# Performance work log

Measured on AMD Instinct MI355X. Metric: run time of the kernel, lower is better.

Reference implementation:

```python
import jax, jax.numpy as jnp
import numpy as np

N_QUBITS = 16
DIM = 1 << N_QUBITS
NUM_CLASSES = 23
BATCH = 64

# PauliZ sign table: wire 0 is the most-significant bit of the flattened index.
_idx = np.arange(DIM)
SIGNS = np.stack([1 - 2 * ((_idx >> (N_QUBITS - 1 - w)) & 1) for w in range(N_QUBITS)], axis=1).astype(np.float32)  # (DIM, 16)


def _rx_mat(theta):
    c = jnp.cos(theta / 2).astype(jnp.complex64)
    s = (-1j * jnp.sin(theta / 2)).astype(jnp.complex64)
    return jnp.stack([jnp.stack([c, s]), jnp.stack([s, c])])  # (2,2)


def _rot_mat(phi, theta, omega):
    ct = jnp.cos(theta / 2)
    st = jnp.sin(theta / 2)
    a = jnp.exp(-0.5j * (phi + omega)) * ct
    b = -jnp.exp(0.5j * (phi - omega)) * st
    c = jnp.exp(-0.5j * (phi - omega)) * st
    d = jnp.exp(0.5j * (phi + omega)) * ct
    return jnp.stack([jnp.stack([a, b]), jnp.stack([c, d])]).astype(jnp.complex64)


def _apply_1q(state, U, w):
    # state: (B, 2,...,2); shared 2x2 gate on wire w (axis w+1)
    st = jnp.tensordot(state, U, axes=[[w + 1], [1]])  # contracted axis moves to last
    return jnp.moveaxis(st, -1, w + 1)


def _apply_rx_batched(state, theta_b, w):
    # per-sample RX angles theta_b: (B,)
    half = theta_b / 2
    c = jnp.cos(half).astype(jnp.complex64)
    s = (-1j * jnp.sin(half)).astype(jnp.complex64)
    U = jnp.stack([jnp.stack([c, s], -1), jnp.stack([s, c], -1)], -2)  # (B,2,2)
    st = jnp.moveaxis(state, w + 1, -1)
    st = jnp.einsum('bji,b...i->b...j', U, st)
    return jnp.moveaxis(st, -1, w + 1)


def _apply_crx(state, theta, ctrl, tgt):
    s0 = jax.lax.index_in_dim(state, 0, axis=ctrl + 1, keepdims=False)
    s1 = jax.lax.index_in_dim(state, 1, axis=ctrl + 1, keepdims=False)
    tax = tgt + 1 if tgt < ctrl else tgt  # target axis after control axis removal
    U = _rx_mat(theta)
    s1 = jnp.moveaxis(jnp.tensordot(s1, U, axes=[[tax], [1]]), -1, tax)
    return jnp.stack([s0, s1], axis=ctrl + 1)


def _circuit(x, w0, x0, w1, x1):
    B = x.shape[0]
    state = jnp.zeros((B,) + (2,) * N_QUBITS, jnp.complex64)
    state = state.at[(slice(None),) + (0,) * N_QUBITS].set(1.0)
    for w, xc in ((w0, x0), (w1, x1)):
        for q in range(N_QUBITS):
            state = _apply_rx_batched(state, x[:, q], q)
        for q in range(N_QUBITS):
            state = _apply_1q(state, _rot_mat(w[q, 0], w[q, 1], w[q, 2]), q)
        for q in range(N_QUBITS):
            state = _apply_crx(state, xc[q], q, (q + 1) % N_QUBITS)
    probs = (state.real ** 2 + state.imag ** 2).reshape(B, DIM)
    return probs @ jnp.asarray(SIGNS)  # (B, 16) PauliZ expvals


def setup_inputs() -> dict:
    key = jax.random.key(0)
    ks = jax.random.split(key, 7)
    return {
        'x': jax.random.normal(ks[0], (BATCH, N_QUBITS), jnp.float32),
        'w0': jax.random.normal(ks[1], (N_QUBITS, 3), jnp.float32),
        'x0': jax.random.normal(ks[2], (N_QUBITS,), jnp.float32),
        'w1': jax.random.normal(ks[3], (N_QUBITS, 3), jnp.float32),
        'x1': jax.random.normal(ks[4], (N_QUBITS,), jnp.float32),
        'fc_w': jax.random.normal(ks[5], (NUM_CLASSES, N_QUBITS), jnp.float32) * 0.25,
        'fc_b': jax.random.normal(ks[6], (NUM_CLASSES,), jnp.float32) * 0.05,
    }


def reference(x, w0, x0, w1, x1, fc_w, fc_b):
    feats = _circuit(x, w0, x0, w1, x1)           # (B, 16)
    logits = feats @ fc_w.T + fc_b                # (B, 23)
    return jax.nn.log_softmax(logits, axis=1)
```

## Files before the change

### kernel.cpp

```cpp
#include <hip/hip_runtime.h>
#include <hip/hip_bf16.h>


#define DIM 65536
#define BATCH 64
#define PSTR 580


template<int RB>
__device__ __forceinline__ void g1q_reg(float* sr, float* si, const float* U) {
  float u00r=U[0],u00i=U[1],u01r=U[2],u01i=U[3],u10r=U[4],u10i=U[5],u11r=U[6],u11i=U[7];
#pragma unroll
  for (int k = 0; k < 8; ++k) {
    int lo = k & ((1<<RB)-1);
    int j0 = ((k >> RB) << (RB+1)) | lo;
    int j1 = j0 | (1<<RB);
    float a0r=sr[j0], a0i=si[j0], a1r=sr[j1], a1i=si[j1];
    sr[j0] = u00r*a0r - u00i*a0i + u01r*a1r - u01i*a1i;
    si[j0] = u00r*a0i + u00i*a0r + u01r*a1i + u01i*a1r;
    sr[j1] = u10r*a0r - u10i*a0i + u11r*a1r - u11i*a1i;
    si[j1] = u10r*a0i + u10i*a0r + u11r*a1i + u11i*a1r;
  }
}

template<int RB, int CB>
__device__ __forceinline__ void gsel_reg_cc(float* sr, float* si, const float* M0, const float* M1) {
  float a0=M0[0],a1=M0[1],a2=M0[2],a3=M0[3],a4=M0[4],a5=M0[5],a6=M0[6],a7=M0[7];
  float b0=M1[0],b1=M1[1],b2=M1[2],b3=M1[3],b4=M1[4],b5=M1[5],b6=M1[6],b7=M1[7];
#pragma unroll
  for (int k = 0; k < 8; ++k) {
    int lo = k & ((1<<RB)-1);
    int j0 = ((k >> RB) << (RB+1)) | lo;
    int j1 = j0 | (1<<RB);
    const bool c = ((j0 >> CB) & 1) != 0;
    float u00r=c?b0:a0, u00i=c?b1:a1, u01r=c?b2:a2, u01i=c?b3:a3;
    float u10r=c?b4:a4, u10i=c?b5:a5, u11r=c?b6:a6, u11i=c?b7:a7;
    float p0r=sr[j0], p0i=si[j0], p1r=sr[j1], p1i=si[j1];
    sr[j0] = u00r*p0r - u00i*p0i + u01r*p1r - u01i*p1i;
    si[j0] = u00r*p0i + u00i*p0r + u01r*p1i + u01i*p1r;
    sr[j1] = u10r*p0r - u10i*p0i + u11r*p1r - u11i*p1i;
    si[j1] = u10r*p0i + u10i*p0r + u11r*p1i + u11i*p1r;
  }
}

template<int RB>
__device__ __forceinline__ void gsel_reg_pred(float* sr, float* si, const float* M0,
                                              const float* M1, bool ctrl) {
  float u[8];
#pragma unroll
  for (int e = 0; e < 8; ++e) u[e] = ctrl ? M1[e] : M0[e];
  g1q_reg<RB>(sr, si, u);
}

template<int CB, int LB>
__device__ __forceinline__ void crx_reg_lane(float* sr, float* si, float c, float s) {
#pragma unroll
  for (int k = 0; k < 8; ++k) {
    int lo2 = k & ((1<<CB)-1);
    int j = ((((k >> CB) << (CB+1)) | lo2)) | (1<<CB);
    float pr = __shfl_xor(sr[j], 1<<LB, 64);
    float pi = __shfl_xor(si[j], 1<<LB, 64);
    float mr = sr[j], mi = si[j];
    sr[j] = c*mr + s*pi;
    si[j] = c*mi - s*pr;
  }
}

__device__ __forceinline__ int swz(int o) { return o ^ ((o>>4)&15) ^ ((o>>8)&15); }

__device__ __forceinline__ unsigned bfp(float r, float i) {
  unsigned ur = __float_as_uint(r), ui = __float_as_uint(i);
  ur = (ur + 0x7fffu + ((ur >> 16) & 1u)) >> 16;
  ui = (ui + 0x7fffu + ((ui >> 16) & 1u)) & 0xffff0000u;
  return (ur & 0xffffu) | ui;
}
__device__ __forceinline__ float bfr(unsigned u) { return __uint_as_float(u << 16); }
__device__ __forceinline__ float bfi(unsigned u) { return __uint_as_float(u & 0xffff0000u); }

#define MP(Pb, l, q, s) ((Pb) + (((l)*16+(q))*2+(s))*8)


__global__ __launch_bounds__(256) void pA(float2* __restrict__ pre2, float* __restrict__ P,
                                          const float* __restrict__ x, const float* __restrict__ w0,
                                          const float* __restrict__ x0, const float* __restrict__ w1,
                                          const float* __restrict__ x1, float* __restrict__ feats,
                                          int* __restrict__ ctr) {
  __shared__ float2 lds2[4096];
  int b = blockIdx.x;
  int t = threadIdx.x, lane = t & 63, wv = t >> 6;
  float* Pb = P + (size_t)b * PSTR;

  {
    float (*su)[8] = reinterpret_cast<float(*)[8]>(lds2);
    if (t < 16) feats[b*16 + t] = 0.f;
    if (t == 16) ctr[b] = 0;
    if (t < 32) {
      int l = t >> 4, q = t & 15;
      const float* W = (l ? w1 : w0) + q*3;
      float xa = 0.5f * x[b*16 + q];
      float cr = cosf(xa), sx = sinf(xa);
      float phi = W[0], th = W[1], om = W[2];
      float ct = cosf(0.5f*th), stt = sinf(0.5f*th);
      float po = 0.5f*(phi+om), pm = 0.5f*(phi-om);
      float ar =  cosf(po)*ct,  ai = -sinf(po)*ct;
      float br = -cosf(pm)*stt, bi = -sinf(pm)*stt;
      float cr2 = cosf(pm)*stt, ci2 = -sinf(pm)*stt;
      float dr =  cosf(po)*ct,  di =  sinf(po)*ct;
      float U[8];
      U[0] = ar*cr + bi*sx;   U[1] = ai*cr - br*sx;
      U[2] = ai*sx + br*cr;   U[3] = -ar*sx + bi*cr;
      U[4] = cr2*cr + di*sx;  U[5] = ci2*cr - dr*sx;
      U[6] = ci2*sx + dr*cr;  U[7] = -cr2*sx + di*cr;
      float* M0 = MP(Pb, l, q, 0);
      float* M1 = M0 + 8;
#pragma unroll
      for (int e = 0; e < 8; ++e) { M0[e] = U[e]; su[t][e] = U[e]; }
      if (q == 0) {
        float ang = l ? 0.5f*x0[15] : 0.f;
        float cg = cosf(ang), sg = sinf(ang);
        M1[0] =  cg*U[0] + sg*U[3];  M1[1] = cg*U[1] - sg*U[2];
        M1[2] =  sg*U[1] + cg*U[2];  M1[3] = -sg*U[0] + cg*U[3];
        M1[4] =  cg*U[4] + sg*U[7];  M1[5] = cg*U[5] - sg*U[6];
        M1[6] =  sg*U[5] + cg*U[6];  M1[7] = -sg*U[4] + cg*U[7];
      } else {
        float ang = 0.5f*(l ? x1[q-1] : x0[q-1]);
        float cg = cosf(ang), sg = sinf(ang);
        M1[0] = cg*U[0] + sg*U[5];  M1[1] = cg*U[1] - sg*U[4];
        M1[2] = cg*U[2] + sg*U[7];  M1[3] = cg*U[3] - sg*U[6];
        M1[4] = cg*U[4] + sg*U[1];  M1[5] = cg*U[5] - sg*U[0];
        M1[6] = cg*U[6] + sg*U[3];  M1[7] = cg*U[7] - sg*U[2];
      }
      if (t == 0) { Pb[576] = cosf(0.5f*x1[15]); Pb[577] = sinf(0.5f*x1[15]); }
    }
    __syncthreads();
    if (t == 0) {
      float T0r[8], T0i[8], T1r[8], T1i[8];
#pragma unroll
      for (int k = 0; k < 8; ++k) {
        int b2 = (k>>2)&1, b1 = (k>>1)&1, b0k = k&1;
        float xr = su[13][b2*4], xi = su[13][b2*4+1];
        float yr = su[14][b1*4], yi = su[14][b1*4+1];
        float zr = su[15][b0k*4], zi = su[15][b0k*4+1];
        float pr = xr*yr - xi*yi, pi = xr*yi + xi*yr;
        T0r[k] = pr*zr - pi*zi; T0i[k] = pr*zi + pi*zr;
      }
      float a12 = 0.5f*x0[12], c12 = cosf(a12), s12 = sinf(a12);
#pragma unroll
      for (int k = 0; k < 8; ++k) { T1r[k] = c12*T0r[k] + s12*T0i[k^4]; T1i[k] = c12*T0i[k] - s12*T0r[k^4]; }
      float a13 = 0.5f*x0[13], c13 = cosf(a13), s13 = sinf(a13);
      float n0r[8], n0i[8], n1r[8], n1i[8];
#pragma unroll
      for (int k = 0; k < 8; ++k) {
        if (k & 4) {
          n0r[k] = c13*T0r[k] + s13*T0i[k^2]; n0i[k] = c13*T0i[k] - s13*T0r[k^2];
          n1r[k] = c13*T1r[k] + s13*T1i[k^2]; n1i[k] = c13*T1i[k] - s13*T1r[k^2];
        } else { n0r[k]=T0r[k]; n0i[k]=T0i[k]; n1r[k]=T1r[k]; n1i[k]=T1i[k]; }
      }
      float a14 = 0.5f*x0[14], c14 = cosf(a14), s14 = sinf(a14);
      float Fr[2][8], Fi[2][8];
#pragma unroll
      for (int k = 0; k < 8; ++k) {
        float r0, i0, r1, i1;
        if (k & 2) {
          r0 = c14*n0r[k] + s14*n0i[k^1]; i0 = c14*n0i[k] - s14*n0r[k^1];
          r1 = c14*n1r[k] + s14*n1i[k^1]; i1 = c14*n1i[k] - s14*n1r[k^1];
        } else { r0=n0r[k]; i0=n0i[k]; r1=n1r[k]; i1=n1i[k]; }
        Fr[0][k] = r0; Fi[0][k] = i0; Fr[1][k] = r1; Fi[1][k] = i1;
      }
      const float* A = MP(Pb,0,12,0);
      const float* B = MP(Pb,0,12,1);
      float wr[2][2], wi[2][2];
      wr[0][0] = A[0]; wi[0][0] = A[1];  wr[1][0] = A[4]; wi[1][0] = A[5];
      wr[0][1] = B[0]; wi[0][1] = B[1];  wr[1][1] = B[4]; wi[1][1] = B[5];
      float* T2 = Pb + 512;
#pragma unroll
      for (int j0 = 0; j0 < 2; ++j0)
#pragma unroll
        for (int j1 = 0; j1 < 2; ++j1)
#pragma unroll
          for (int k = 0; k < 8; ++k) {
            float tr = Fr[j0][k], ti = Fi[j0][k];
            float fr = wr[j0][j1], fi = wi[j0][j1];
            T2[((j0*2 + j1)*8 + k)*2 + 0] = tr*fr - ti*fi;
            T2[((j0*2 + j1)*8 + k)*2 + 1] = tr*fi + ti*fr;
          }
    }
  }

  float sr[16], si[16];
#pragma unroll
  for (int r = 0; r < 16; ++r) { sr[r] = 0.f; si[r] = 0.f; }
  if (t == 0) sr[0] = 1.f;

  g1q_reg<3>(sr, si, MP(Pb,0,0,0));
  gsel_reg_cc<2,3>(sr, si, MP(Pb,0,1,0), MP(Pb,0,1,1));
  gsel_reg_cc<1,2>(sr, si, MP(Pb,0,2,0), MP(Pb,0,2,1));
  gsel_reg_cc<0,1>(sr, si, MP(Pb,0,3,0), MP(Pb,0,3,1));
  __syncthreads();
#pragma unroll
  for (int r = 0; r < 16; ++r) {
    int o = wv | (lane << 2) | (r << 8);
    lds2[swz(o) & 4095] = make_float2(sr[r], si[r]);
  }
  __syncthreads();
#pragma unroll
  for (int r = 0; r < 16; ++r) {
    int o = wv | (((lane>>4)&3) << 2) | (r << 4) | ((lane&15) << 8);
    float2 v = lds2[swz(o) & 4095]; sr[r] = v.x; si[r] = v.y;
  }
  gsel_reg_pred<3>(sr, si, MP(Pb,0,4,0), MP(Pb,0,4,1), (lane&1)!=0);
  gsel_reg_cc<2,3>(sr, si, MP(Pb,0,5,0), MP(Pb,0,5,1));
  gsel_reg_cc<1,2>(sr, si, MP(Pb,0,6,0), MP(Pb,0,6,1));
  gsel_reg_cc<0,1>(sr, si, MP(Pb,0,7,0), MP(Pb,0,7,1));
  __syncthreads();
#pragma unroll
  for (int r = 0; r < 16; ++r) {
    int o = wv | (((lane>>4)&3) << 2) | (r << 4) | ((lane&15) << 8);
    lds2[swz(o) & 4095] = make_float2(sr[r], si[r]);
  }
  __syncthreads();
#pragma unroll
  for (int r = 0; r < 16; ++r) {
    int o = r | (lane << 4) | (wv << 10);
    float2 v = lds2[swz(o) & 4095]; sr[r] = v.x; si[r] = v.y;
  }
  gsel_reg_pred<3>(sr, si, MP(Pb,0,8,0), MP(Pb,0,8,1), (lane&1)!=0);
  gsel_reg_cc<2,3>(sr, si, MP(Pb,0,9,0), MP(Pb,0,9,1));
  gsel_reg_cc<1,2>(sr, si, MP(Pb,0,10,0), MP(Pb,0,10,1));
  gsel_reg_cc<0,1>(sr, si, MP(Pb,0,11,0), MP(Pb,0,11,1));
#pragma unroll
  for (int r = 0; r < 16; ++r) {
    int paddr = ((lane>>4)&3) | (wv << 2) | (r << 4) | ((lane&15) << 8);
    pre2[(size_t)b*4096 + paddr] = make_float2(sr[r], si[r]);
  }
}


__global__ __launch_bounds__(512) void pB(unsigned* __restrict__ st, const float2* __restrict__ pre2,
                                          const float* __restrict__ P) {
  __shared__ float2 lds2[8192];
  int blk = blockIdx.x;
  int b = blk >> 3, m = blk & 7;
  int t = threadIdx.x, lane = t & 63, wv = t >> 6;
  const float* Pb = P + (size_t)b*PSTR;

  float sr[16], si[16];
  {
    const float4* src = (const float4*)(pre2 + (size_t)b*4096) + ((lane << 3) | ((wv&3) << 9));
    int k = ((wv>>2)&1) | ((m&3) << 1);
    const float* tf = Pb + 512 + ((((m>>2)&1)*2 + (lane&1))*8 + k)*2;
    float fr = tf[0], fi = tf[1];
#pragma unroll
    for (int g = 0; g < 8; ++g) {
      float4 v = src[g];
      sr[2*g]   = fr*v.x - fi*v.y;  si[2*g]   = fr*v.y + fi*v.x;
      sr[2*g+1] = fr*v.z - fi*v.w;  si[2*g+1] = fr*v.w + fi*v.z;
    }
  }
  gsel_reg_pred<3>(sr, si, MP(Pb,1,0,0), MP(Pb,1,0,1), ((wv>>2)&1)!=0);
  gsel_reg_cc<2,3>(sr, si, MP(Pb,1,1,0), MP(Pb,1,1,1));
  gsel_reg_cc<1,2>(sr, si, MP(Pb,1,2,0), MP(Pb,1,2,1));
  gsel_reg_cc<0,1>(sr, si, MP(Pb,1,3,0), MP(Pb,1,3,1));
#pragma unroll
  for (int r = 0; r < 16; ++r) {
    int o = (lane&63) | ((wv&3) << 6) | (r << 8) | (((wv>>2)&1) << 12);
    lds2[swz(o) & 8191] = make_float2(sr[r], si[r]);
  }
  __syncthreads();
#pragma unroll
  for (int r = 0; r < 16; ++r) {
    int o = (lane&15) | (r << 4) | (((lane>>4)&3) << 8) | ((wv&3) << 10) | (((wv>>2)&1) << 12);
    float2 v = lds2[swz(o) & 8191]; sr[r] = v.x; si[r] = v.y;
  }
  gsel_reg_pred<3>(sr, si, MP(Pb,1,4,0), MP(Pb,1,4,1), (lane&16)!=0);
  gsel_reg_cc<2,3>(sr, si, MP(Pb,1,5,0), MP(Pb,1,5,1));
  gsel_reg_cc<1,2>(sr, si, MP(Pb,1,6,0), MP(Pb,1,6,1));
  gsel_reg_cc<0,1>(sr, si, MP(Pb,1,7,0), MP(Pb,1,7,1));
  __syncthreads();
#pragma unroll
  for (int r = 0; r < 16; ++r) {
    int o = (lane&15) | (r << 4) | (((lane>>4)&3) << 8) | ((wv&3) << 10) | (((wv>>2)&1) << 12);
    lds2[swz(o) & 8191] = make_float2(sr[r], si[r]);
  }
  __syncthreads();
#pragma unroll
  for (int r = 0; r < 16; ++r) {
    int o = r | ((lane&63) << 4) | ((wv&3) << 10) | (((wv>>2)&1) << 12);
    float2 v = lds2[swz(o) & 8191]; sr[r] = v.x; si[r] = v.y;
  }
  gsel_reg_pred<3>(sr, si, MP(Pb,1,8,0), MP(Pb,1,8,1), (lane&1)!=0);
  gsel_reg_cc<2,3>(sr, si, MP(Pb,1,9,0), MP(Pb,1,9,1));
  gsel_reg_cc<1,2>(sr, si, MP(Pb,1,10,0), MP(Pb,1,10,1));
  gsel_reg_cc<0,1>(sr, si, MP(Pb,1,11,0), MP(Pb,1,11,1));
  {
    int sbase = ((lane&63) << 4) | ((wv&3) << 10) | (((wv>>2)&1) << 12) | (m << 13);
    uint4* dst = (uint4*)(st + (size_t)b*DIM + sbase);
#pragma unroll
    for (int g = 0; g < 4; ++g)
      dst[g] = make_uint4(bfp(sr[4*g],si[4*g]), bfp(sr[4*g+1],si[4*g+1]),
                          bfp(sr[4*g+2],si[4*g+2]), bfp(sr[4*g+3],si[4*g+3]));
  }
}


__global__ __launch_bounds__(512) void p3(const unsigned* __restrict__ st, const float* __restrict__ P,
                                          float* __restrict__ feats, int* __restrict__ ctr,
                                          const float* __restrict__ fcw, const float* __restrict__ fcb,
                                          float* __restrict__ out) {
  int blk = blockIdx.x;
  int b = blk >> 3, n = blk & 7;
  int t = threadIdx.x, lane = t & 63, wv = t >> 6;
  const float* Pb = P + (size_t)b*PSTR;
  int base = (lane&31) | (wv << 5) | (n << 8) | ((lane>>5) << 11);
  const unsigned* S = st + (size_t)b*DIM + base;
  float sr[16], si[16];
#pragma unroll
  for (int r = 0; r < 16; ++r) { unsigned u = S[r << 12]; sr[r] = bfr(u); si[r] = bfi(u); }

  gsel_reg_pred<3>(sr, si, MP(Pb,1,12,0), MP(Pb,1,12,1), (lane&1)!=0);
  gsel_reg_cc<2,3>(sr, si, MP(Pb,1,13,0), MP(Pb,1,13,1));
  gsel_reg_cc<1,2>(sr, si, MP(Pb,1,14,0), MP(Pb,1,14,1));
  gsel_reg_cc<0,1>(sr, si, MP(Pb,1,15,0), MP(Pb,1,15,1));
  crx_reg_lane<0,5>(sr, si, Pb[576], Pb[577]);

  float tot=0.f, sA=0.f, sB=0.f, sC=0.f, sD=0.f;
#pragma unroll
  for (int r = 0; r < 16; ++r) {
    float p = sr[r]*sr[r] + si[r]*si[r];
    tot += p;
    sA += (r & 1) ? -p : p;
    sB += (r & 2) ? -p : p;
    sC += (r & 4) ? -p : p;
    sD += (r & 8) ? -p : p;
  }
  float f[16];
  f[15] = sA; f[14] = sB; f[13] = sC; f[12] = sD;
  f[11] = (lane&1)  ? -tot : tot;
  f[10] = (lane&2)  ? -tot : tot;
  f[9]  = (lane&4)  ? -tot : tot;
  f[8]  = (lane&8)  ? -tot : tot;
  f[7]  = (lane&16) ? -tot : tot;
  f[0]  = (lane&32) ? -tot : tot;
  f[6]  = (wv&1)    ? -tot : tot;
  f[5]  = (wv&2)    ? -tot : tot;
  f[4]  = (wv&4)    ? -tot : tot;
  f[3]  = (n&1)     ? -tot : tot;
  f[2]  = (n&2)     ? -tot : tot;
  f[1]  = (n&4)     ? -tot : tot;
#pragma unroll
  for (int w = 0; w < 16; ++w) {
#pragma unroll
    for (int off = 32; off; off >>= 1) f[w] += __shfl_xor(f[w], off, 64);
  }
  __shared__ float red[8][17];
  if (lane == 0) {
#pragma unroll
    for (int w = 0; w < 16; ++w) red[wv][w] = f[w];
  }
  __syncthreads();
  if (t < 16) {
    float acc = 0.f;
#pragma unroll
    for (int i = 0; i < 8; ++i) acc += red[i][t];
    atomicAdd(&feats[b*16 + t], acc);
  }

  __shared__ int flagS;
  __syncthreads();
  if (t == 0) { __threadfence(); flagS = atomicAdd(&ctr[b], 1); }
  __syncthreads();
  if (flagS == 7) {
    __shared__ float fs[16];
    __shared__ float lg[23];
    if (t < 16) fs[t] = __hip_atomic_load(&feats[b*16 + t], __ATOMIC_RELAXED, __HIP_MEMORY_SCOPE_AGENT);
    __syncthreads();
    if (t < 23) {
      float acc = fcb[t];
#pragma unroll
      for (int w = 0; w < 16; ++w) acc += fs[w] * fcw[t*16 + w];
      lg[t] = acc;
    }
    __syncthreads();
    if (t < 23) {
      float mx = -1e30f;
#pragma unroll
      for (int j = 0; j < 23; ++j) mx = fmaxf(mx, lg[j]);
      float Ssum = 0.f;
#pragma unroll
      for (int j = 0; j < 23; ++j) Ssum += expf(lg[j] - mx);
      out[b*23 + t] = lg[t] - mx - logf(Ssum);
    }
  }
}

extern "C" void kernel_launch(void* const* d_in, const int* in_sizes, int n_in,
                              void* d_out, int out_size, void* d_ws, size_t ws_size,
                              hipStream_t stream) {
  const float* x   = (const float*)d_in[0];
  const float* w0  = (const float*)d_in[1];
  const float* x0  = (const float*)d_in[2];
  const float* w1  = (const float*)d_in[3];
  const float* x1  = (const float*)d_in[4];
  const float* fcw = (const float*)d_in[5];
  const float* fcb = (const float*)d_in[6];
  float* out = (float*)d_out;

  char* ws = (char*)d_ws;
  unsigned* st  = (unsigned*)ws;
  float2* pre2  = (float2*)(ws + (size_t)BATCH * DIM * 4);
  float*  P     = (float*)((char*)pre2 + (size_t)BATCH * 4096 * 8);
  float*  feats = P + (size_t)BATCH * PSTR;
  int*    ctr   = (int*)(feats + BATCH*16);

  pA<<<BATCH, 256, 0, stream>>>(pre2, P, x, w0, x0, w1, x1, feats, ctr);
  pB<<<512, 512, 0, stream>>>(st, pre2, P);
  p3<<<512, 512, 0, stream>>>(st, P, feats, ctr, fcw, fcb, out);
  (void)in_sizes; (void)n_in; (void)out_size; (void)ws_size;
}
```

Before: 125.7 us.

## Fuse three kernels into one cooperative kernel with grid syncs

Merges the three launches into a single cooperative kernel of 256 blocks. Grid-wide syncs now separate the stages, and each block handles two work units in the later stages. This removes two kernel launches and the per-batch atomic counter used to pick the block that runs the final softmax. It also folds the prefactor multiply into the first gate matrix. The costs are three grid.sync barriers, half as many blocks in the main phases, and only 256 of 512 threads working during the first stage.

```diff
diff --git a/kernel.cpp b/kernel.cpp
--- a/kernel.cpp
+++ b/kernel.cpp
@@ -1,11 +1,13 @@
 #include <hip/hip_runtime.h>
 #include <hip/hip_bf16.h>
-
+#include <hip/hip_cooperative_groups.h>
+
+
+namespace cg = cooperative_groups;
 
 #define DIM 65536
 #define BATCH 64
 #define PSTR 580
-
 
 template<int RB>
 __device__ __forceinline__ void g1q_reg(float* sr, float* si, const float* U) {
@@ -79,299 +81,306 @@
 
 #define MP(Pb, l, q, s) ((Pb) + (((l)*16+(q))*2+(s))*8)
 
-
-__global__ __launch_bounds__(256) void pA(float2* __restrict__ pre2, float* __restrict__ P,
-                                          const float* __restrict__ x, const float* __restrict__ w0,
-                                          const float* __restrict__ x0, const float* __restrict__ w1,
-                                          const float* __restrict__ x1, float* __restrict__ feats,
-                                          int* __restrict__ ctr) {
-  __shared__ float2 lds2[4096];
-  int b = blockIdx.x;
+__global__ __launch_bounds__(512) void uber(
+    const float* __restrict__ x, const float* __restrict__ w0, const float* __restrict__ x0,
+    const float* __restrict__ w1, const float* __restrict__ x1, const float* __restrict__ fcw,
+    const float* __restrict__ fcb, float* __restrict__ out, unsigned* __restrict__ st,
+    float2* __restrict__ pre2, float* __restrict__ P, float* __restrict__ feats) {
+  cg::grid_group grid = cg::this_grid();
+  __shared__ float2 lds2[8192];
+  __shared__ float red[8][17];
+  __shared__ float fs[16];
+  __shared__ float lg[23];
+  int blk = blockIdx.x;
   int t = threadIdx.x, lane = t & 63, wv = t >> 6;
-  float* Pb = P + (size_t)b * PSTR;
-
-  {
-    float (*su)[8] = reinterpret_cast<float(*)[8]>(lds2);
-    if (t < 16) feats[b*16 + t] = 0.f;
-    if (t == 16) ctr[b] = 0;
-    if (t < 32) {
-      int l = t >> 4, q = t & 15;
-      const float* W = (l ? w1 : w0) + q*3;
-      float xa = 0.5f * x[b*16 + q];
-      float cr = cosf(xa), sx = sinf(xa);
-      float phi = W[0], th = W[1], om = W[2];
-      float ct = cosf(0.5f*th), stt = sinf(0.5f*th);
-      float po = 0.5f*(phi+om), pm = 0.5f*(phi-om);
-      float ar =  cosf(po)*ct,  ai = -sinf(po)*ct;
-      float br = -cosf(pm)*stt, bi = -sinf(pm)*stt;
-      float cr2 = cosf(pm)*stt, ci2 = -sinf(pm)*stt;
-      float dr =  cosf(po)*ct,  di =  sinf(po)*ct;
-      float U[8];
-      U[0] = ar*cr + bi*sx;   U[1] = ai*cr - br*sx;
-      U[2] = ai*sx + br*cr;   U[3] = -ar*sx + bi*cr;
-      U[4] = cr2*cr + di*sx;  U[5] = ci2*cr - dr*sx;
-      U[6] = ci2*sx + dr*cr;  U[7] = -cr2*sx + di*cr;
-      float* M0 = MP(Pb, l, q, 0);
-      float* M1 = M0 + 8;
-#pragma unroll
-      for (int e = 0; e < 8; ++e) { M0[e] = U[e]; su[t][e] = U[e]; }
-      if (q == 0) {
-        float ang = l ? 0.5f*x0[15] : 0.f;
-        float cg = cosf(ang), sg = sinf(ang);
-        M1[0] =  cg*U[0] + sg*U[3];  M1[1] = cg*U[1] - sg*U[2];
-        M1[2] =  sg*U[1] + cg*U[2];  M1[3] = -sg*U[0] + cg*U[3];
-        M1[4] =  cg*U[4] + sg*U[7];  M1[5] = cg*U[5] - sg*U[6];
-        M1[6] =  sg*U[5] + cg*U[6];  M1[7] = -sg*U[4] + cg*U[7];
-      } else {
-        float ang = 0.5f*(l ? x1[q-1] : x0[q-1]);
-        float cg = cosf(ang), sg = sinf(ang);
-        M1[0] = cg*U[0] + sg*U[5];  M1[1] = cg*U[1] - sg*U[4];
-        M1[2] = cg*U[2] + sg*U[7];  M1[3] = cg*U[3] - sg*U[6];
-        M1[4] = cg*U[4] + sg*U[1];  M1[5] = cg*U[5] - sg*U[0];
-        M1[6] = cg*U[6] + sg*U[3];  M1[7] = cg*U[7] - sg*U[2];
-      }
-      if (t == 0) { Pb[576] = cosf(0.5f*x1[15]); Pb[577] = sinf(0.5f*x1[15]); }
-    }
-    __syncthreads();
-    if (t == 0) {
-      float T0r[8], T0i[8], T1r[8], T1i[8];
-#pragma unroll
-      for (int k = 0; k < 8; ++k) {
-        int b2 = (k>>2)&1, b1 = (k>>1)&1, b0k = k&1;
-        float xr = su[13][b2*4], xi = su[13][b2*4+1];
-        float yr = su[14][b1*4], yi = su[14][b1*4+1];
-        float zr = su[15][b0k*4], zi = su[15][b0k*4+1];
-        float pr = xr*yr - xi*yi, pi = xr*yi + xi*yr;
-        T0r[k] = pr*zr - pi*zi; T0i[k] = pr*zi + pi*zr;
-      }
-      float a12 = 0.5f*x0[12], c12 = cosf(a12), s12 = sinf(a12);
-#pragma unroll
-      for (int k = 0; k < 8; ++k) { T1r[k] = c12*T0r[k] + s12*T0i[k^4]; T1i[k] = c12*T0i[k] - s12*T0r[k^4]; }
-      float a13 = 0.5f*x0[13], c13 = cosf(a13), s13 = sinf(a13);
-      float n0r[8], n0i[8], n1r[8], n1i[8];
-#pragma unroll
-      for (int k = 0; k < 8; ++k) {
-        if (k & 4) {
-          n0r[k] = c13*T0r[k] + s13*T0i[k^2]; n0i[k] = c13*T0i[k] - s13*T0r[k^2];
-          n1r[k] = c13*T1r[k] + s13*T1i[k^2]; n1i[k] = c13*T1i[k] - s13*T1r[k^2];
-        } else { n0r[k]=T0r[k]; n0i[k]=T0i[k]; n1r[k]=T1r[k]; n1i[k]=T1i[k]; }
-      }
-      float a14 = 0.5f*x0[14], c14 = cosf(a14), s14 = sinf(a14);
-      float Fr[2][8], Fi[2][8];
-#pragma unroll
-      for (int k = 0; k < 8; ++k) {
-        float r0, i0, r1, i1;
-        if (k & 2) {
-          r0 = c14*n0r[k] + s14*n0i[k^1]; i0 = c14*n0i[k] - s14*n0r[k^1];
-          r1 = c14*n1r[k] + s14*n1i[k^1]; i1 = c14*n1i[k] - s14*n1r[k^1];
-        } else { r0=n0r[k]; i0=n0i[k]; r1=n1r[k]; i1=n1i[k]; }
-        Fr[0][k] = r0; Fi[0][k] = i0; Fr[1][k] = r1; Fi[1][k] = i1;
-      }
-      const float* A = MP(Pb,0,12,0);
-      const float* B = MP(Pb,0,12,1);
-      float wr[2][2], wi[2][2];
-      wr[0][0] = A[0]; wi[0][0] = A[1];  wr[1][0] = A[4]; wi[1][0] = A[5];
-      wr[0][1] = B[0]; wi[0][1] = B[1];  wr[1][1] = B[4]; wi[1][1] = B[5];
-      float* T2 = Pb + 512;
-#pragma unroll
-      for (int j0 = 0; j0 < 2; ++j0)
-#pragma unroll
-        for (int j1 = 0; j1 < 2; ++j1)
-#pragma unroll
-          for (int k = 0; k < 8; ++k) {
-            float tr = Fr[j0][k], ti = Fi[j0][k];
-            float fr = wr[j0][j1], fi = wi[j0][j1];
-            T2[((j0*2 + j1)*8 + k)*2 + 0] = tr*fr - ti*fi;
-            T2[((j0*2 + j1)*8 + k)*2 + 1] = tr*fi + ti*fr;
-          }
-    }
-  }
-
-  float sr[16], si[16];
-#pragma unroll
-  for (int r = 0; r < 16; ++r) { sr[r] = 0.f; si[r] = 0.f; }
-  if (t == 0) sr[0] = 1.f;
-
-  g1q_reg<3>(sr, si, MP(Pb,0,0,0));
-  gsel_reg_cc<2,3>(sr, si, MP(Pb,0,1,0), MP(Pb,0,1,1));
-  gsel_reg_cc<1,2>(sr, si, MP(Pb,0,2,0), MP(Pb,0,2,1));
-  gsel_reg_cc<0,1>(sr, si, MP(Pb,0,3,0), MP(Pb,0,3,1));
-  __syncthreads();
-#pragma unroll
-  for (int r = 0; r < 16; ++r) {
-    int o = wv | (lane << 2) | (r << 8);
-    lds2[swz(o) & 4095] = make_float2(sr[r], si[r]);
-  }
-  __syncthreads();
-#pragma unroll
-  for (int r = 0; r < 16; ++r) {
-    int o = wv | (((lane>>4)&3) << 2) | (r << 4) | ((lane&15) << 8);
-    float2 v = lds2[swz(o) & 4095]; sr[r] = v.x; si[r] = v.y;
-  }
-  gsel_reg_pred<3>(sr, si, MP(Pb,0,4,0), MP(Pb,0,4,1), (lane&1)!=0);
-  gsel_reg_cc<2,3>(sr, si, MP(Pb,0,5,0), MP(Pb,0,5,1));
-  gsel_reg_cc<1,2>(sr, si, MP(Pb,0,6,0), MP(Pb,0,6,1));
-  gsel_reg_cc<0,1>(sr, si, MP(Pb,0,7,0), MP(Pb,0,7,1));
-  __syncthreads();
-#pragma unroll
-  for (int r = 0; r < 16; ++r) {
-    int o = wv | (((lane>>4)&3) << 2) | (r << 4) | ((lane&15) << 8);
-    lds2[swz(o) & 4095] = make_float2(sr[r], si[r]);
-  }
-  __syncthreads();
-#pragma unroll
-  for (int r = 0; r < 16; ++r) {
-    int o = r | (lane << 4) | (wv << 10);
-    float2 v = lds2[swz(o) & 4095]; sr[r] = v.x; si[r] = v.y;
-  }
-  gsel_reg_pred<3>(sr, si, MP(Pb,0,8,0), MP(Pb,0,8,1), (lane&1)!=0);
-  gsel_reg_cc<2,3>(sr, si, MP(Pb,0,9,0), MP(Pb,0,9,1));
-  gsel_reg_cc<1,2>(sr, si, MP(Pb,0,10,0), MP(Pb,0,10,1));
-  gsel_reg_cc<0,1>(sr, si, MP(Pb,0,11,0), MP(Pb,0,11,1));
-#pragma unroll
-  for (int r = 0; r < 16; ++r) {
-    int paddr = ((lane>>4)&3) | (wv << 2) | (r << 4) | ((lane&15) << 8);
-    pre2[(size_t)b*4096 + paddr] = make_float2(sr[r], si[r]);
-  }
-}
-
-
-__global__ __launch_bounds__(512) void pB(unsigned* __restrict__ st, const float2* __restrict__ pre2,
-                                          const float* __restrict__ P) {
-  __shared__ float2 lds2[8192];
-  int blk = blockIdx.x;
-  int b = blk >> 3, m = blk & 7;
-  int t = threadIdx.x, lane = t & 63, wv = t >> 6;
-  const float* Pb = P + (size_t)b*PSTR;
-
-  float sr[16], si[16];
-  {
-    const float4* src = (const float4*)(pre2 + (size_t)b*4096) + ((lane << 3) | ((wv&3) << 9));
-    int k = ((wv>>2)&1) | ((m&3) << 1);
-    const float* tf = Pb + 512 + ((((m>>2)&1)*2 + (lane&1))*8 + k)*2;
-    float fr = tf[0], fi = tf[1];
-#pragma unroll
-    for (int g = 0; g < 8; ++g) {
-      float4 v = src[g];
-      sr[2*g]   = fr*v.x - fi*v.y;  si[2*g]   = fr*v.y + fi*v.x;
-      sr[2*g+1] = fr*v.z - fi*v.w;  si[2*g+1] = fr*v.w + fi*v.z;
-    }
-  }
-  gsel_reg_pred<3>(sr, si, MP(Pb,1,0,0), MP(Pb,1,0,1), ((wv>>2)&1)!=0);
-  gsel_reg_cc<2,3>(sr, si, MP(Pb,1,1,0), MP(Pb,1,1,1));
-  gsel_reg_cc<1,2>(sr, si, MP(Pb,1,2,0), MP(Pb,1,2,1));
-  gsel_reg_cc<0,1>(sr, si, MP(Pb,1,3,0), MP(Pb,1,3,1));
-#pragma unroll
-  for (int r = 0; r < 16; ++r) {
-    int o = (lane&63) | ((wv&3) << 6) | (r << 8) | (((wv>>2)&1) << 12);
-    lds2[swz(o) & 8191] = make_float2(sr[r], si[r]);
-  }
-  __syncthreads();
-#pragma unroll
-  for (int r = 0; r < 16; ++r) {
-    int o = (lane&15) | (r << 4) | (((lane>>4)&3) << 8) | ((wv&3) << 10) | (((wv>>2)&1) << 12);
-    float2 v = lds2[swz(o) & 8191]; sr[r] = v.x; si[r] = v.y;
-  }
-  gsel_reg_pred<3>(sr, si, MP(Pb,1,4,0), MP(Pb,1,4,1), (lane&16)!=0);
-  gsel_reg_cc<2,3>(sr, si, MP(Pb,1,5,0), MP(Pb,1,5,1));
-  gsel_reg_cc<1,2>(sr, si, MP(Pb,1,6,0), MP(Pb,1,6,1));
-  gsel_reg_cc<0,1>(sr, si, MP(Pb,1,7,0), MP(Pb,1,7,1));
-  __syncthreads();
-#pragma unroll
-  for (int r = 0; r < 16; ++r) {
-    int o = (lane&15) | (r << 4) | (((lane>>4)&3) << 8) | ((wv&3) << 10) | (((wv>>2)&1) << 12);
-    lds2[swz(o) & 8191] = make_float2(sr[r], si[r]);
-  }
-  __syncthreads();
-#pragma unroll
-  for (int r = 0; r < 16; ++r) {
-    int o = r | ((lane&63) << 4) | ((wv&3) << 10) | (((wv>>2)&1) << 12);
-    float2 v = lds2[swz(o) & 8191]; sr[r] = v.x; si[r] = v.y;
-  }
-  gsel_reg_pred<3>(sr, si, MP(Pb,1,8,0), MP(Pb,1,8,1), (lane&1)!=0);
-  gsel_reg_cc<2,3>(sr, si, MP(Pb,1,9,0), MP(Pb,1,9,1));
-  gsel_reg_cc<1,2>(sr, si, MP(Pb,1,10,0), MP(Pb,1,10,1));
-  gsel_reg_cc<0,1>(sr, si, MP(Pb,1,11,0), MP(Pb,1,11,1));
-  {
-    int sbase = ((lane&63) << 4) | ((wv&3) << 10) | (((wv>>2)&1) << 12) | (m << 13);
-    uint4* dst = (uint4*)(st + (size_t)b*DIM + sbase);
-#pragma unroll
-    for (int g = 0; g < 4; ++g)
-      dst[g] = make_uint4(bfp(sr[4*g],si[4*g]), bfp(sr[4*g+1],si[4*g+1]),
-                          bfp(sr[4*g+2],si[4*g+2]), bfp(sr[4*g+3],si[4*g+3]));
-  }
-}
-
-
-__global__ __launch_bounds__(512) void p3(const unsigned* __restrict__ st, const float* __restrict__ P,
-                                          float* __restrict__ feats, int* __restrict__ ctr,
-                                          const float* __restrict__ fcw, const float* __restrict__ fcb,
-                                          float* __restrict__ out) {
-  int blk = blockIdx.x;
-  int b = blk >> 3, n = blk & 7;
-  int t = threadIdx.x, lane = t & 63, wv = t >> 6;
-  const float* Pb = P + (size_t)b*PSTR;
-  int base = (lane&31) | (wv << 5) | (n << 8) | ((lane>>5) << 11);
-  const unsigned* S = st + (size_t)b*DIM + base;
-  float sr[16], si[16];
-#pragma unroll
-  for (int r = 0; r < 16; ++r) { unsigned u = S[r << 12]; sr[r] = bfr(u); si[r] = bfi(u); }
-
-  gsel_reg_pred<3>(sr, si, MP(Pb,1,12,0), MP(Pb,1,12,1), (lane&1)!=0);
-  gsel_reg_cc<2,3>(sr, si, MP(Pb,1,13,0), MP(Pb,1,13,1));
-  gsel_reg_cc<1,2>(sr, si, MP(Pb,1,14,0), MP(Pb,1,14,1));
-  gsel_reg_cc<0,1>(sr, si, MP(Pb,1,15,0), MP(Pb,1,15,1));
-  crx_reg_lane<0,5>(sr, si, Pb[576], Pb[577]);
-
-  float tot=0.f, sA=0.f, sB=0.f, sC=0.f, sD=0.f;
-#pragma unroll
-  for (int r = 0; r < 16; ++r) {
-    float p = sr[r]*sr[r] + si[r]*si[r];
-    tot += p;
-    sA += (r & 1) ? -p : p;
-    sB += (r & 2) ? -p : p;
-    sC += (r & 4) ? -p : p;
-    sD += (r & 8) ? -p : p;
-  }
-  float f[16];
-  f[15] = sA; f[14] = sB; f[13] = sC; f[12] = sD;
-  f[11] = (lane&1)  ? -tot : tot;
-  f[10] = (lane&2)  ? -tot : tot;
-  f[9]  = (lane&4)  ? -tot : tot;
-  f[8]  = (lane&8)  ? -tot : tot;
-  f[7]  = (lane&16) ? -tot : tot;
-  f[0]  = (lane&32) ? -tot : tot;
-  f[6]  = (wv&1)    ? -tot : tot;
-  f[5]  = (wv&2)    ? -tot : tot;
-  f[4]  = (wv&4)    ? -tot : tot;
-  f[3]  = (n&1)     ? -tot : tot;
-  f[2]  = (n&2)     ? -tot : tot;
-  f[1]  = (n&4)     ? -tot : tot;
-#pragma unroll
-  for (int w = 0; w < 16; ++w) {
-#pragma unroll
-    for (int off = 32; off; off >>= 1) f[w] += __shfl_xor(f[w], off, 64);
-  }
-  __shared__ float red[8][17];
-  if (lane == 0) {
-#pragma unroll
-    for (int w = 0; w < 16; ++w) red[wv][w] = f[w];
-  }
-  __syncthreads();
-  if (t < 16) {
-    float acc = 0.f;
-#pragma unroll
-    for (int i = 0; i < 8; ++i) acc += red[i][t];
-    atomicAdd(&feats[b*16 + t], acc);
-  }
-
-  __shared__ int flagS;
-  __syncthreads();
-  if (t == 0) { __threadfence(); flagS = atomicAdd(&ctr[b], 1); }
-  __syncthreads();
-  if (flagS == 7) {
-    __shared__ float fs[16];
-    __shared__ float lg[23];
+
+  if (blk < 64) {
+    int b = blk;
+    float* Pb = P + (size_t)b * PSTR;
+    {
+      float (*su)[8] = reinterpret_cast<float(*)[8]>(lds2);
+      if (t < 16) feats[b*16 + t] = 0.f;
+      if (t < 32) {
+        int l = t >> 4, q = t & 15;
+        const float* W = (l ? w1 : w0) + q*3;
+        float xa = 0.5f * x[b*16 + q];
+        float cr = cosf(xa), sx = sinf(xa);
+        float phi = W[0], th = W[1], om = W[2];
+        float ct = cosf(0.5f*th), stt = sinf(0.5f*th);
+        float po = 0.5f*(phi+om), pm = 0.5f*(phi-om);
+        float ar =  cosf(po)*ct,  ai = -sinf(po)*ct;
+        float br = -cosf(pm)*stt, bi = -sinf(pm)*stt;
+        float cr2 = cosf(pm)*stt, ci2 = -sinf(pm)*stt;
+        float dr =  cosf(po)*ct,  di =  sinf(po)*ct;
+        float U[8];
+        U[0] = ar*cr + bi*sx;   U[1] = ai*cr - br*sx;
+        U[2] = ai*sx + br*cr;   U[3] = -ar*sx + bi*cr;
+        U[4] = cr2*cr + di*sx;  U[5] = ci2*cr - dr*sx;
+        U[6] = ci2*sx + dr*cr;  U[7] = -cr2*sx + di*cr;
+        float* M0 = MP(Pb, l, q, 0);
+        float* M1 = M0 + 8;
+#pragma unroll
+        for (int e = 0; e < 8; ++e) { M0[e] = U[e]; su[t][e] = U[e]; }
+        if (q == 0) {
+          float ang = l ? 0.5f*x0[15] : 0.f;
+          float cg2 = cosf(ang), sg = sinf(ang);
+          M1[0] =  cg2*U[0] + sg*U[3];  M1[1] = cg2*U[1] - sg*U[2];
+          M1[2] =  sg*U[1] + cg2*U[2];  M1[3] = -sg*U[0] + cg2*U[3];
+          M1[4] =  cg2*U[4] + sg*U[7];  M1[5] = cg2*U[5] - sg*U[6];
+          M1[6] =  sg*U[5] + cg2*U[6];  M1[7] = -sg*U[4] + cg2*U[7];
+        } else {
+          float ang = 0.5f*(l ? x1[q-1] : x0[q-1]);
+          float cg2 = cosf(ang), sg = sinf(ang);
+          M1[0] = cg2*U[0] + sg*U[5];  M1[1] = cg2*U[1] - sg*U[4];
+          M1[2] = cg2*U[2] + sg*U[7];  M1[3] = cg2*U[3] - sg*U[6];
+          M1[4] = cg2*U[4] + sg*U[1];  M1[5] = cg2*U[5] - sg*U[0];
+          M1[6] = cg2*U[6] + sg*U[3];  M1[7] = cg2*U[7] - sg*U[2];
+        }
+        if (t == 0) { Pb[576] = cosf(0.5f*x1[15]); Pb[577] = sinf(0.5f*x1[15]); }
+      }
+      __syncthreads();
+      if (t == 0) {
+        float T0r[8], T0i[8], T1r[8], T1i[8];
+#pragma unroll
+        for (int k = 0; k < 8; ++k) {
+          int b2 = (k>>2)&1, b1 = (k>>1)&1, b0k = k&1;
+          float xr = su[13][b2*4], xi = su[13][b2*4+1];
+          float yr = su[14][b1*4], yi = su[14][b1*4+1];
+          float zr = su[15][b0k*4], zi = su[15][b0k*4+1];
+          float pr = xr*yr - xi*yi, pi = xr*yi + xi*yr;
+          T0r[k] = pr*zr - pi*zi; T0i[k] = pr*zi + pi*zr;
+        }
+        float a12 = 0.5f*x0[12], c12 = cosf(a12), s12 = sinf(a12);
+#pragma unroll
+        for (int k = 0; k < 8; ++k) { T1r[k] = c12*T0r[k] + s12*T0i[k^4]; T1i[k] = c12*T0i[k] - s12*T0r[k^4]; }
+        float a13 = 0.5f*x0[13], c13 = cosf(a13), s13 = sinf(a13);
+        float n0r[8], n0i[8], n1r[8], n1i[8];
+#pragma unroll
+        for (int k = 0; k < 8; ++k) {
+          if (k & 4) {
+            n0r[k] = c13*T0r[k] + s13*T0i[k^2]; n0i[k] = c13*T0i[k] - s13*T0r[k^2];
+            n1r[k] = c13*T1r[k] + s13*T1i[k^2]; n1i[k] = c13*T1i[k] - s13*T1r[k^2];
+          } else { n0r[k]=T0r[k]; n0i[k]=T0i[k]; n1r[k]=T1r[k]; n1i[k]=T1i[k]; }
+        }
+        float a14 = 0.5f*x0[14], c14 = cosf(a14), s14 = sinf(a14);
+        float Fr[2][8], Fi[2][8];
+#pragma unroll
+        for (int k = 0; k < 8; ++k) {
+          float r0, i0, r1, i1;
+          if (k & 2) {
+            r0 = c14*n0r[k] + s14*n0i[k^1]; i0 = c14*n0i[k] - s14*n0r[k^1];
+            r1 = c14*n1r[k] + s14*n1i[k^1]; i1 = c14*n1i[k] - s14*n1r[k^1];
+          } else { r0=n0r[k]; i0=n0i[k]; r1=n1r[k]; i1=n1i[k]; }
+          Fr[0][k] = r0; Fi[0][k] = i0; Fr[1][k] = r1; Fi[1][k] = i1;
+        }
+        const float* A = MP(Pb,0,12,0);
+        const float* B = MP(Pb,0,12,1);
+        float wr[2][2], wi[2][2];
+        wr[0][0] = A[0]; wi[0][0] = A[1];  wr[1][0] = A[4]; wi[1][0] = A[5];
+        wr[0][1] = B[0]; wi[0][1] = B[1];  wr[1][1] = B[4]; wi[1][1] = B[5];
+        float* T2 = Pb + 512;
+#pragma unroll
+        for (int j0 = 0; j0 < 2; ++j0)
+#pragma unroll
+          for (int j1 = 0; j1 < 2; ++j1)
+#pragma unroll
+            for (int k = 0; k < 8; ++k) {
+              float tr = Fr[j0][k], ti = Fi[j0][k];
+              float fr = wr[j0][j1], fi = wi[j0][j1];
+              T2[((j0*2 + j1)*8 + k)*2 + 0] = tr*fr - ti*fi;
+              T2[((j0*2 + j1)*8 + k)*2 + 1] = tr*fi + ti*fr;
+            }
+      }
+      __syncthreads();
+    }
+    float sr[16], si[16];
+    if (t < 256) {
+#pragma unroll
+      for (int r = 0; r < 16; ++r) { sr[r] = 0.f; si[r] = 0.f; }
+      if (t == 0) sr[0] = 1.f;
+      g1q_reg<3>(sr, si, MP(Pb,0,0,0));
+      gsel_reg_cc<2,3>(sr, si, MP(Pb,0,1,0), MP(Pb,0,1,1));
+      gsel_reg_cc<1,2>(sr, si, MP(Pb,0,2,0), MP(Pb,0,2,1));
+      gsel_reg_cc<0,1>(sr, si, MP(Pb,0,3,0), MP(Pb,0,3,1));
+#pragma unroll
+      for (int r = 0; r < 16; ++r) {
+        int o = wv | (lane << 2) | (r << 8);
+        lds2[swz(o) & 4095] = make_float2(sr[r], si[r]);
+      }
+    }
+    __syncthreads();
+    if (t < 256) {
+#pragma unroll
+      for (int r = 0; r < 16; ++r) {
+        int o = wv | (((lane>>4)&3) << 2) | (r << 4) | ((lane&15) << 8);
+        float2 v = lds2[swz(o) & 4095]; sr[r] = v.x; si[r] = v.y;
+      }
+      gsel_reg_pred<3>(sr, si, MP(Pb,0,4,0), MP(Pb,0,4,1), (lane&1)!=0);
+      gsel_reg_cc<2,3>(sr, si, MP(Pb,0,5,0), MP(Pb,0,5,1));
+      gsel_reg_cc<1,2>(sr, si, MP(Pb,0,6,0), MP(Pb,0,6,1));
+      gsel_reg_cc<0,1>(sr, si, MP(Pb,0,7,0), MP(Pb,0,7,1));
+    }
+    __syncthreads();
+    if (t < 256) {
+#pragma unroll
+      for (int r = 0; r < 16; ++r) {
+        int o = wv | (((lane>>4)&3) << 2) | (r << 4) | ((lane&15) << 8);
+        lds2[swz(o) & 4095] = make_float2(sr[r], si[r]);
+      }
+    }
+    __syncthreads();
+    if (t < 256) {
+#pragma unroll
+      for (int r = 0; r < 16; ++r) {
+        int o = r | (lane << 4) | (wv << 10);
+        float2 v = lds2[swz(o) & 4095]; sr[r] = v.x; si[r] = v.y;
+      }
+      gsel_reg_pred<3>(sr, si, MP(Pb,0,8,0), MP(Pb,0,8,1), (lane&1)!=0);
+      gsel_reg_cc<2,3>(sr, si, MP(Pb,0,9,0), MP(Pb,0,9,1));
+      gsel_reg_cc<1,2>(sr, si, MP(Pb,0,10,0), MP(Pb,0,10,1));
+      gsel_reg_cc<0,1>(sr, si, MP(Pb,0,11,0), MP(Pb,0,11,1));
+#pragma unroll
+      for (int r = 0; r < 16; ++r) {
+        int paddr = ((lane>>4)&3) | (wv << 2) | (r << 4) | ((lane&15) << 8);
+        pre2[(size_t)b*4096 + paddr] = make_float2(sr[r], si[r]);
+      }
+    }
+  }
+  grid.sync();
+
+#pragma unroll 1
+  for (int u = 0; u < 2; ++u) {
+    int wu = blk + u*256;
+    int b = wu >> 3, m = wu & 7;
+    const float* Pb = P + (size_t)b*PSTR;
+    float sr[16], si[16];
+    __syncthreads();
+    {
+      const float4* src = (const float4*)(pre2 + (size_t)b*4096) + ((lane << 3) | ((wv&3) << 9));
+      int k = ((wv>>2)&1) | ((m&3) << 1);
+      const float* tf = Pb + 512 + ((((m>>2)&1)*2 + (lane&1))*8 + k)*2;
+      float fr = tf[0], fi = tf[1];
+#pragma unroll
+      for (int g = 0; g < 8; ++g) {
+        float4 v = src[g];
+        sr[2*g] = v.x; si[2*g] = v.y; sr[2*g+1] = v.z; si[2*g+1] = v.w;
+      }
+      const float* M = ((wv>>2)&1) ? MP(Pb,1,0,1) : MP(Pb,1,0,0);
+      float v8[8];
+#pragma unroll
+      for (int e = 0; e < 4; ++e) {
+        v8[2*e]   = fr*M[2*e] - fi*M[2*e+1];
+        v8[2*e+1] = fr*M[2*e+1] + fi*M[2*e];
+      }
+      g1q_reg<3>(sr, si, v8);
+    }
+    gsel_reg_cc<2,3>(sr, si, MP(Pb,1,1,0), MP(Pb,1,1,1));
+    gsel_reg_cc<1,2>(sr, si, MP(Pb,1,2,0), MP(Pb,1,2,1));
+    gsel_reg_cc<0,1>(sr, si, MP(Pb,1,3,0), MP(Pb,1,3,1));
+#pragma unroll
+    for (int r = 0; r < 16; ++r) {
+      int o = (lane&63) | ((wv&3) << 6) | (r << 8) | (((wv>>2)&1) << 12);
+      lds2[swz(o) & 8191] = make_float2(sr[r], si[r]);
+    }
+    __syncthreads();
+#pragma unroll
+    for (int r = 0; r < 16; ++r) {
+      int o = (lane&15) | (r << 4) | (((lane>>4)&3) << 8) | ((wv&3) << 10) | (((wv>>2)&1) << 12);
+      float2 v = lds2[swz(o) & 8191]; sr[r] = v.x; si[r] = v.y;
+    }
+    gsel_reg_pred<3>(sr, si, MP(Pb,1,4,0), MP(Pb,1,4,1), (lane&16)!=0);
+    gsel_reg_cc<2,3>(sr, si, MP(Pb,1,5,0), MP(Pb,1,5,1));
+    gsel_reg_cc<1,2>(sr, si, MP(Pb,1,6,0), MP(Pb,1,6,1));
+    gsel_reg_cc<0,1>(sr, si, MP(Pb,1,7,0), MP(Pb,1,7,1));
+    __syncthreads();
+#pragma unroll
+    for (int r = 0; r < 16; ++r) {
+      int o = (lane&15) | (r << 4) | (((lane>>4)&3) << 8) | ((wv&3) << 10) | (((wv>>2)&1) << 12);
+      lds2[swz(o) & 8191] = make_float2(sr[r], si[r]);
+    }
+    __syncthreads();
+#pragma unroll
+    for (int r = 0; r < 16; ++r) {
+      int o = r | ((lane&63) << 4) | ((wv&3) << 10) | (((wv>>2)&1) << 12);
+      float2 v = lds2[swz(o) & 8191]; sr[r] = v.x; si[r] = v.y;
+    }
+    gsel_reg_pred<3>(sr, si, MP(Pb,1,8,0), MP(Pb,1,8,1), (lane&1)!=0);
+    gsel_reg_cc<2,3>(sr, si, MP(Pb,1,9,0), MP(Pb,1,9,1));
+    gsel_reg_cc<1,2>(sr, si, MP(Pb,1,10,0), MP(Pb,1,10,1));
+    gsel_reg_cc<0,1>(sr, si, MP(Pb,1,11,0), MP(Pb,1,11,1));
+    {
+      int sbase = ((lane&63) << 4) | ((wv&3) << 10) | (((wv>>2)&1) << 12) | (m << 13);
+      uint4* dst = (uint4*)(st + (size_t)b*DIM + sbase);
+#pragma unroll
+      for (int g = 0; g < 4; ++g)
+        dst[g] = make_uint4(bfp(sr[4*g],si[4*g]), bfp(sr[4*g+1],si[4*g+1]),
+                            bfp(sr[4*g+2],si[4*g+2]), bfp(sr[4*g+3],si[4*g+3]));
+    }
+  }
+  grid.sync();
+
+#pragma unroll 1
+  for (int u = 0; u < 2; ++u) {
+    int wu = blk + u*256;
+    int b = wu >> 3, n = wu & 7;
+    const float* Pb = P + (size_t)b*PSTR;
+    int base = (lane&31) | (wv << 5) | (n << 8) | ((lane>>5) << 11);
+    const unsigned* S = st + (size_t)b*DIM + base;
+    float sr[16], si[16];
+#pragma unroll
+    for (int r = 0; r < 16; ++r) { unsigned uu = S[r << 12]; sr[r] = bfr(uu); si[r] = bfi(uu); }
+    gsel_reg_pred<3>(sr, si, MP(Pb,1,12,0), MP(Pb,1,12,1), (lane&1)!=0);
+    gsel_reg_cc<2,3>(sr, si, MP(Pb,1,13,0), MP(Pb,1,13,1));
+    gsel_reg_cc<1,2>(sr, si, MP(Pb,1,14,0), MP(Pb,1,14,1));
+    gsel_reg_cc<0,1>(sr, si, MP(Pb,1,15,0), MP(Pb,1,15,1));
+    crx_reg_lane<0,5>(sr, si, Pb[576], Pb[577]);
+
+    float tot=0.f, sA=0.f, sB=0.f, sC=0.f, sD=0.f;
+#pragma unroll
+    for (int r = 0; r < 16; ++r) {
+      float p = sr[r]*sr[r] + si[r]*si[r];
+      tot += p;
+      sA += (r & 1) ? -p : p;
+      sB += (r & 2) ? -p : p;
+      sC += (r & 4) ? -p : p;
+      sD += (r & 8) ? -p : p;
+    }
+    float f[16];
+    f[15] = sA; f[14] = sB; f[13] = sC; f[12] = sD;
+    f[11] = (lane&1)  ? -tot : tot;
+    f[10] = (lane&2)  ? -tot : tot;
+    f[9]  = (lane&4)  ? -tot : tot;
+    f[8]  = (lane&8)  ? -tot : tot;
+    f[7]  = (lane&16) ? -tot : tot;
+    f[0]  = (lane&32) ? -tot : tot;
+    f[6]  = (wv&1)    ? -tot : tot;
+    f[5]  = (wv&2)    ? -tot : tot;
+    f[4]  = (wv&4)    ? -tot : tot;
+    f[3]  = (n&1)     ? -tot : tot;
+    f[2]  = (n&2)     ? -tot : tot;
+    f[1]  = (n&4)     ? -tot : tot;
+#pragma unroll
+    for (int w = 0; w < 16; ++w) {
+#pragma unroll
+      for (int off = 32; off; off >>= 1) f[w] += __shfl_xor(f[w], off, 64);
+    }
+    __syncthreads();
+    if (lane == 0) {
+#pragma unroll
+      for (int w = 0; w < 16; ++w) red[wv][w] = f[w];
+    }
+    __syncthreads();
+    if (t < 16) {
+      float acc = 0.f;
+#pragma unroll
+      for (int i = 0; i < 8; ++i) acc += red[i][t];
+      atomicAdd(&feats[b*16 + t], acc);
+    }
+  }
+  grid.sync();
+
+  if (blk < 64) {
+    int b = blk;
     if (t < 16) fs[t] = __hip_atomic_load(&feats[b*16 + t], __ATOMIC_RELAXED, __HIP_MEMORY_SCOPE_AGENT);
     __syncthreads();
     if (t < 23) {
@@ -410,10 +419,10 @@
   float2* pre2  = (float2*)(ws + (size_t)BATCH * DIM * 4);
   float*  P     = (float*)((char*)pre2 + (size_t)BATCH * 4096 * 8);
   float*  feats = P + (size_t)BATCH * PSTR;
-  int*    ctr   = (int*)(feats + BATCH*16);
-
-  pA<<<BATCH, 256, 0, stream>>>(pre2, P, x, w0, x0, w1, x1, feats, ctr);
-  pB<<<512, 512, 0, stream>>>(st, pre2, P);
-  p3<<<512, 512, 0, stream>>>(st, P, feats, ctr, fcw, fcb, out);
+
+  void* args[] = { (void*)&x, (void*)&w0, (void*)&x0, (void*)&w1, (void*)&x1,
+                   (void*)&fcw, (void*)&fcb, (void*)&out, (void*)&st, (void*)&pre2,
+                   (void*)&P, (void*)&feats };
+  hipLaunchCooperativeKernel((const void*)uber, dim3(256), dim3(512), args, 0, stream);
   (void)in_sizes; (void)n_in; (void)out_size; (void)ws_size;
 }
```

Result: slower. 221.6 us (+76.4%).
